# Optimization experiments

Hardware: AMD Instinct MI355X
Metric: run time of the kernel (lower is better)

Reference implementation:

```python
import jax, jax.numpy as jnp
import numpy as np

DIM = 512

def setup_inputs() -> dict:
    key = jax.random.key(0)
    k1, k2 = jax.random.split(key)
    pq = jax.random.normal(k1, (65536, 2 * DIM), dtype=jnp.float32)
    A = jax.random.normal(k2, (DIM, DIM), dtype=jnp.float32)
    return {"pq": pq, "A": A}

def reference(pq, A):
    # up_or_low == 'up': p' = p + (A + A^T) q ; q' = q
    S = A + A.T  # symmetric (dim, dim)
    p = pq[..., :DIM]
    q = pq[..., DIM:]
    # (A+A^T) q for each row: since S is symmetric, q @ S == q @ S^T
    pterm = jnp.einsum('bd,ed->be', q, S)  # matches mv(S, q) per row
    return jnp.concatenate([p + pterm, q], axis=-1)
```

## Files before the change

kernel.cpp:

```cpp
#include <hip/hip_runtime.h>
#include <hip/hip_bf16.h>

#define DIM 512
#define BM 64
#define BK 32
#define LSTRIDE 40

typedef __bf16 bf16x8 __attribute__((ext_vector_type(8)));
typedef float f32x16 __attribute__((ext_vector_type(16)));

union B128 { uint4 u; bf16x8 v; };

__device__ __forceinline__ unsigned short f2bf(float f) {
    union { __hip_bfloat16 b; unsigned short u; } c;
    c.b = __float2bfloat16(f);
    return c.u;
}

__global__ void prep_s_kernel(const float* __restrict__ A,
                              unsigned short* __restrict__ S) {
    int i = blockIdx.x * 256 + threadIdx.x;
    int e = i >> 9;
    int d = i & 511;
    S[i] = f2bf(A[e * DIM + d] + A[d * DIM + e]);
}

__global__ __launch_bounds__(512, 4) void fused_gemm_kernel(
        const float* __restrict__ pq,
        const unsigned short* __restrict__ S,
        float* __restrict__ out) {
    __shared__ __align__(16) unsigned short qs[BM * LSTRIDE];
    __shared__ __align__(16) unsigned short ss[DIM * LSTRIDE];

    const int t = threadIdx.x;
    const int l = t & 63;
    const int w = t >> 6;
    const int wm = w >> 2;
    const int wn = w & 3;
    const int half = l >> 5;
    const int lane31 = l & 31;
    const int m0 = blockIdx.x * BM;

    f32x16 acc[4];
    #pragma unroll
    for (int nt = 0; nt < 4; ++nt)
        #pragma unroll
        for (int r = 0; r < 16; ++r) acc[nt][r] = 0.0f;

    const int qrow = t >> 3;
    const int qcol = (t & 7) * 4;

    for (int kc = 0; kc < DIM / BK; ++kc) {
        const int k0 = kc * BK;

        const size_t qoff = (size_t)(m0 + qrow) * (2 * DIM) + DIM + k0 + qcol;
        float4 qv = *(const float4*)(pq + qoff);
        *(float4*)(out + qoff) = qv;

        if (kc) __syncthreads();

        ushort4 qb;
        qb.x = f2bf(qv.x); qb.y = f2bf(qv.y); qb.z = f2bf(qv.z); qb.w = f2bf(qv.w);
        *(ushort4*)&qs[qrow * LSTRIDE + qcol] = qb;

        #pragma unroll
        for (int i = 0; i < 4; ++i) {
            int ch = i * 512 + t;
            int srow = ch >> 2;
            int scol = (ch & 3) * 8;
            uint4 sv = *(const uint4*)(S + (size_t)srow * DIM + k0 + scol);
            *(uint4*)&ss[srow * LSTRIDE + scol] = sv;
        }
        __syncthreads();

        B128 a0, a1;
        const int arow = 32 * wm + lane31;
        a0.u = *(const uint4*)&qs[arow * LSTRIDE + half * 8];
        a1.u = *(const uint4*)&qs[arow * LSTRIDE + 16 + half * 8];
        #pragma unroll
        for (int nt = 0; nt < 4; ++nt) {
            const int brow = 128 * nt + 32 * wn + lane31;
            B128 b0, b1;
            b0.u = *(const uint4*)&ss[brow * LSTRIDE + half * 8];
            b1.u = *(const uint4*)&ss[brow * LSTRIDE + 16 + half * 8];
            acc[nt] = __builtin_amdgcn_mfma_f32_32x32x16_bf16(a0.v, b0.v, acc[nt], 0, 0, 0);
            acc[nt] = __builtin_amdgcn_mfma_f32_32x32x16_bf16(a1.v, b1.v, acc[nt], 0, 0, 0);
        }
    }

    #pragma unroll
    for (int nt = 0; nt < 4; ++nt) {
        const int col = 128 * nt + 32 * wn + lane31;
        #pragma unroll
        for (int r = 0; r < 16; ++r) {
            const int row = m0 + 32 * wm + 4 * half + (r & 3) + 8 * (r >> 2);
            const size_t off = (size_t)row * (2 * DIM) + col;
            out[off] = pq[off] + acc[nt][r];
        }
    }
}

extern "C" void kernel_launch(void* const* d_in, const int* in_sizes, int n_in,
                              void* d_out, int out_size, void* d_ws, size_t ws_size,
                              hipStream_t stream) {
    const float* pq = (const float*)d_in[0];
    const float* A  = (const float*)d_in[1];
    float* out = (float*)d_out;
    unsigned short* S = (unsigned short*)d_ws;

    prep_s_kernel<<<(DIM * DIM) / 256, 256, 0, stream>>>(A, S);
    fused_gemm_kernel<<<65536 / BM, 512, 0, stream>>>(pq, S, out);
}
```

Baseline: 524.6 us.

## Pre-swizzle S into MFMA fragment layout and stage full Q tile once

The prep kernel now writes S+S^T in bf16 directly in the per-lane MFMA B-fragment order, so the GEMM loads B fragments straight from global/L2 with no LDS staging. The whole 64x512 q tile is converted to bf16 and stored in LDS once, in a swizzled fragment layout, which removes the per-k-chunk barriers. The epilogue stages accumulators through LDS so the p-add reads and output writes use coalesced float4 accesses. The cost is 64KB of LDS per block, which limits occupancy, and B operands now come from L2 on every k step.

```diff
diff --git a/kernel.cpp b/kernel.cpp
--- a/kernel.cpp
+++ b/kernel.cpp
@@ -3,8 +3,6 @@
 
 #define DIM 512
 #define BM 64
-#define BK 32
-#define LSTRIDE 40
 
 typedef __bf16 bf16x8 __attribute__((ext_vector_type(8)));
 typedef float f32x16 __attribute__((ext_vector_type(16)));
@@ -18,28 +16,61 @@
 }
 
 __global__ void prep_s_kernel(const float* __restrict__ A,
-                              unsigned short* __restrict__ S) {
-    int i = blockIdx.x * 256 + threadIdx.x;
-    int e = i >> 9;
-    int d = i & 511;
-    S[i] = f2bf(A[e * DIM + d] + A[d * DIM + e]);
+                              unsigned short* __restrict__ Sf) {
+    const int c   = blockIdx.x * 256 + threadIdx.x;
+    const int l   = c & 63;
+    const int ks  = (c >> 6) & 31;
+    const int nt2 = c >> 11;
+    const int e   = nt2 * 32 + (l & 31);
+    const int d0  = ks * 16 + (l >> 5) * 8;
+    float4 r0 = *(const float4*)(A + (size_t)e * DIM + d0);
+    float4 r1 = *(const float4*)(A + (size_t)e * DIM + d0 + 4);
+    float cl[8];
+    #pragma unroll
+    for (int j = 0; j < 8; ++j) cl[j] = A[(size_t)(d0 + j) * DIM + e];
+    ushort4 o0, o1;
+    o0.x = f2bf(r0.x + cl[0]); o0.y = f2bf(r0.y + cl[1]);
+    o0.z = f2bf(r0.z + cl[2]); o0.w = f2bf(r0.w + cl[3]);
+    o1.x = f2bf(r1.x + cl[4]); o1.y = f2bf(r1.y + cl[5]);
+    o1.z = f2bf(r1.z + cl[6]); o1.w = f2bf(r1.w + cl[7]);
+    *(ushort4*)(Sf + (size_t)c * 8)     = o0;
+    *(ushort4*)(Sf + (size_t)c * 8 + 4) = o1;
 }
 
 __global__ __launch_bounds__(512, 4) void fused_gemm_kernel(
         const float* __restrict__ pq,
-        const unsigned short* __restrict__ S,
+        const unsigned short* __restrict__ Sf,
         float* __restrict__ out) {
-    __shared__ __align__(16) unsigned short qs[BM * LSTRIDE];
-    __shared__ __align__(16) unsigned short ss[DIM * LSTRIDE];
+    __shared__ __align__(16) unsigned char smem[65536];
+    unsigned short* As = (unsigned short*)smem;
+    float*          Cs = (float*)smem;
 
-    const int t = threadIdx.x;
-    const int l = t & 63;
-    const int w = t >> 6;
+    const int t  = threadIdx.x;
+    const int l  = t & 63;
+    const int w  = t >> 6;
     const int wm = w >> 2;
     const int wn = w & 3;
-    const int half = l >> 5;
     const int lane31 = l & 31;
+    const int half   = l >> 5;
     const int m0 = blockIdx.x * BM;
+
+    #pragma unroll 4
+    for (int p = 0; p < 16; ++p) {
+        const int u   = p * 512 + t;
+        const int row = u >> 7;
+        const int col = (u & 127) * 4;
+        const size_t goff = (size_t)(m0 + row) * (2 * DIM) + DIM + col;
+        float4 qv = *(const float4*)(pq + goff);
+        *(float4*)(out + goff) = qv;
+        ushort4 qb;
+        qb.x = f2bf(qv.x); qb.y = f2bf(qv.y); qb.z = f2bf(qv.z); qb.w = f2bf(qv.w);
+        const int mt   = row >> 5;
+        const int ks   = col >> 4;
+        const int lpos = (row & 31) + ((col >> 3) & 1) * 32;
+        const int chunk = (mt * 32 + ks) * 64 + (lpos ^ (ks & 7));
+        *(ushort4*)(As + chunk * 8 + (col & 7)) = qb;
+    }
+    __syncthreads();
 
     f32x16 acc[4];
     #pragma unroll
@@ -47,55 +78,43 @@
         #pragma unroll
         for (int r = 0; r < 16; ++r) acc[nt][r] = 0.0f;
 
-    const int qrow = t >> 3;
-    const int qcol = (t & 7) * 4;
-
-    for (int kc = 0; kc < DIM / BK; ++kc) {
-        const int k0 = kc * BK;
-
-        const size_t qoff = (size_t)(m0 + qrow) * (2 * DIM) + DIM + k0 + qcol;
-        float4 qv = *(const float4*)(pq + qoff);
-        *(float4*)(out + qoff) = qv;
-
-        if (kc) __syncthreads();
-
-        ushort4 qb;
-        qb.x = f2bf(qv.x); qb.y = f2bf(qv.y); qb.z = f2bf(qv.z); qb.w = f2bf(qv.w);
-        *(ushort4*)&qs[qrow * LSTRIDE + qcol] = qb;
-
-        #pragma unroll
-        for (int i = 0; i < 4; ++i) {
-            int ch = i * 512 + t;
-            int srow = ch >> 2;
-            int scol = (ch & 3) * 8;
-            uint4 sv = *(const uint4*)(S + (size_t)srow * DIM + k0 + scol);
-            *(uint4*)&ss[srow * LSTRIDE + scol] = sv;
-        }
-        __syncthreads();
-
-        B128 a0, a1;
-        const int arow = 32 * wm + lane31;
-        a0.u = *(const uint4*)&qs[arow * LSTRIDE + half * 8];
-        a1.u = *(const uint4*)&qs[arow * LSTRIDE + 16 + half * 8];
+    #pragma unroll 2
+    for (int ks = 0; ks < 32; ++ks) {
+        B128 a;
+        const int achunk = (wm * 32 + ks) * 64 + (l ^ (ks & 7));
+        a.u = *(const uint4*)(As + achunk * 8);
         #pragma unroll
         for (int nt = 0; nt < 4; ++nt) {
-            const int brow = 128 * nt + 32 * wn + lane31;
-            B128 b0, b1;
-            b0.u = *(const uint4*)&ss[brow * LSTRIDE + half * 8];
-            b1.u = *(const uint4*)&ss[brow * LSTRIDE + 16 + half * 8];
-            acc[nt] = __builtin_amdgcn_mfma_f32_32x32x16_bf16(a0.v, b0.v, acc[nt], 0, 0, 0);
-            acc[nt] = __builtin_amdgcn_mfma_f32_32x32x16_bf16(a1.v, b1.v, acc[nt], 0, 0, 0);
+            const int nt2 = nt * 4 + wn;
+            B128 b;
+            b.u = *(const uint4*)(Sf + (size_t)((nt2 * 32 + ks) * 64 + l) * 8);
+            acc[nt] = __builtin_amdgcn_mfma_f32_32x32x16_bf16(a.v, b.v, acc[nt], 0, 0, 0);
         }
     }
 
     #pragma unroll
-    for (int nt = 0; nt < 4; ++nt) {
-        const int col = 128 * nt + 32 * wn + lane31;
+    for (int h = 0; h < 2; ++h) {
+        __syncthreads();
         #pragma unroll
-        for (int r = 0; r < 16; ++r) {
-            const int row = m0 + 32 * wm + 4 * half + (r & 3) + 8 * (r >> 2);
-            const size_t off = (size_t)row * (2 * DIM) + col;
-            out[off] = pq[off] + acc[nt][r];
+        for (int i = 0; i < 2; ++i) {
+            const int nt = 2 * h + i;
+            const int colb = 128 * i + 32 * wn + lane31;
+            #pragma unroll
+            for (int r = 0; r < 16; ++r) {
+                const int row = 32 * wm + 4 * half + (r & 3) + 8 * (r >> 2);
+                Cs[row * 256 + colb] = acc[nt][r];
+            }
+        }
+        __syncthreads();
+        #pragma unroll
+        for (int i = 0; i < 8; ++i) {
+            const int row = i * 8 + w;
+            const int c0  = l * 4;
+            float4 v = *(const float4*)(Cs + row * 256 + c0);
+            const size_t goff = (size_t)(m0 + row) * (2 * DIM) + 256 * h + c0;
+            float4 pv = *(const float4*)(pq + goff);
+            v.x += pv.x; v.y += pv.y; v.z += pv.z; v.w += pv.w;
+            *(float4*)(out + goff) = v;
         }
     }
 }
@@ -106,8 +125,8 @@
     const float* pq = (const float*)d_in[0];
     const float* A  = (const float*)d_in[1];
     float* out = (float*)d_out;
-    unsigned short* S = (unsigned short*)d_ws;
+    unsigned short* Sf = (unsigned short*)d_ws;
 
-    prep_s_kernel<<<(DIM * DIM) / 256, 256, 0, stream>>>(A, S);
-    fused_gemm_kernel<<<65536 / BM, 512, 0, stream>>>(pq, S, out);
+    prep_s_kernel<<<(DIM * DIM / 8) / 256, 256, 0, stream>>>(A, Sf);
+    fused_gemm_kernel<<<65536 / BM, 512, 0, stream>>>(pq, Sf, out);
 }
```

New measurement: 473.3 us. 1.11x faster.
